# Performance work log

Hardware: AMD Instinct MI355X
Metric: run time of the kernel (lower is better)

## Reference

```python
import jax, jax.numpy as jnp
import numpy as np

NODE_SIZE = 500000
LINK_SIZE = 500
DIM = 128
NORM_P = 1
MARGIN = 1.0
BATCH = 16384


def setup_inputs() -> dict:
    key = jax.random.key(0)
    k1, k2, k3, k4, k5, k6, k7, k8 = jax.random.split(key, 8)
    ur_e = 6.0 / np.sqrt(DIM)
    ur_m = 6.0 / DIM
    node_w = jax.random.uniform(k1, (NODE_SIZE, DIM), jnp.float32, -ur_e, ur_e)
    link_w = jax.random.uniform(k2, (LINK_SIZE, DIM), jnp.float32, -ur_e, ur_e)
    transfer_w = jax.random.uniform(k3, (LINK_SIZE, DIM * DIM), jnp.float32, -ur_m, ur_m)
    sp = jax.random.randint(k4, (BATCH,), 0, NODE_SIZE)
    tp = jax.random.randint(k5, (BATCH,), 0, NODE_SIZE)
    sn = jax.random.randint(k6, (BATCH,), 0, NODE_SIZE)
    tn = jax.random.randint(k7, (BATCH,), 0, NODE_SIZE)
    r = jax.random.randint(k8, (BATCH,), 0, LINK_SIZE)
    return {"node_w": node_w, "link_w": link_w, "transfer_w": transfer_w,
            "sp": sp, "tp": tp, "sn": sn, "tn": tn, "r": r}


def _distance(node_w, link_w, transfer_w, s, r, t):
    # gather embeddings
    s_emb = node_w[s]                      # [B, D]
    t_emb = node_w[t]                      # [B, D]
    r_emb = link_w[r]                      # [B, D]
    M = transfer_w[r].reshape(-1, DIM, DIM)  # [B, D, D]
    # per-sample (1xD)x(DxD) matvec: e @ M
    s_proj = jnp.einsum('bd,bde->be', s_emb, M)
    t_proj = jnp.einsum('bd,bde->be', t_emb, M)
    diff = s_proj + r_emb - t_proj
    if NORM_P == 1:
        return jnp.sum(jnp.abs(diff), axis=1)
    return jnp.sum(jnp.abs(diff) ** NORM_P, axis=1) ** (1.0 / NORM_P)


def reference(node_w, link_w, transfer_w, sp, tp, sn, tn, r):
    pos = _distance(node_w, link_w, transfer_w, sp, r, tp)
    neg = _distance(node_w, link_w, transfer_w, sn, r, tn)
    # MarginRankingLoss with target = -1: max(0, (pos - neg) + margin)
    loss = jnp.maximum(pos - neg + MARGIN, 0.0)
    return jnp.mean(loss)
```

## Files before the change

kernel.cpp:

```cpp
#include <hip/hip_runtime.h>

#define BATCH 16384
#define DIM 128
#define NLINK 500

#define WS_COUNTS 0
#define WS_OFFSETS 512
#define WS_CURSOR 1024
#define WS_BUCKET 1536

__global__ void k_zero(int* wsi, float* out) {
    int t = threadIdx.x;
    wsi[WS_COUNTS + t] = 0;
    if (t == 0) out[0] = 0.0f;
}

__global__ void k_hist(const int* __restrict__ r, int* wsi) {
    int i = blockIdx.x * blockDim.x + threadIdx.x;
    if (i < BATCH) atomicAdd(&wsi[WS_COUNTS + r[i]], 1);
}

__global__ void k_scan(int* wsi) {
    __shared__ int buf[512];
    int t = threadIdx.x;
    int v = (t < NLINK) ? wsi[WS_COUNTS + t] : 0;
    buf[t] = v;
    __syncthreads();
    for (int off = 1; off < 512; off <<= 1) {
        int x = (t >= off) ? buf[t - off] : 0;
        __syncthreads();
        buf[t] += x;
        __syncthreads();
    }
    int excl = buf[t] - v;
    if (t < NLINK) {
        wsi[WS_OFFSETS + t] = excl;
        wsi[WS_CURSOR + t] = excl;
    }
    if (t == 0) wsi[WS_OFFSETS + NLINK] = BATCH;
}

__global__ void k_scatter(const int* __restrict__ r, int* wsi) {
    int i = blockIdx.x * blockDim.x + threadIdx.x;
    if (i < BATCH) {
        int pos = atomicAdd(&wsi[WS_CURSOR + r[i]], 1);
        wsi[WS_BUCKET + pos] = i;
    }
}

__global__ __launch_bounds__(256, 2) void k_main(
    const float* __restrict__ node_w, const float* __restrict__ link_w,
    const float* __restrict__ transfer_w,
    const int* __restrict__ sp, const int* __restrict__ tp,
    const int* __restrict__ sn, const int* __restrict__ tn,
    const int* __restrict__ wsi, float* __restrict__ out)
{
    __shared__ float Ms[DIM * DIM];
    __shared__ float dp[8][DIM];
    __shared__ float dn[8][DIM];
    __shared__ float remb[DIM];
    __shared__ float wred[4];

    const int link = blockIdx.x;
    const int t = threadIdx.x;

    {
        const float4* g = (const float4*)(transfer_w + (size_t)link * (DIM * DIM));
        float4* s = (float4*)Ms;
        #pragma unroll
        for (int i = 0; i < 16; i++) s[t + 256 * i] = g[t + 256 * i];
    }
    if (t < 32) ((float4*)remb)[t] = ((const float4*)(link_w + link * DIM))[t];

    const int begin = wsi[WS_OFFSETS + link];
    const int end   = wsi[WS_OFFSETS + link + 1];
    const int sub = t >> 5;
    const int q   = t & 31;

    float loss_acc = 0.0f;
    __syncthreads();

    for (int k = begin; k < end; k += 8) {
        const int myk = k + sub;
        const bool active = (myk < end);
        if (active) {
            int b = wsi[WS_BUCKET + myk];
            const float4* a = (const float4*)(node_w + (size_t)sp[b] * DIM);
            const float4* c = (const float4*)(node_w + (size_t)tp[b] * DIM);
            float4 av = a[q], cv = c[q];
            float4 rp; rp.x = av.x - cv.x; rp.y = av.y - cv.y;
                       rp.z = av.z - cv.z; rp.w = av.w - cv.w;
            ((float4*)dp[sub])[q] = rp;
            const float4* e2 = (const float4*)(node_w + (size_t)sn[b] * DIM);
            const float4* f2 = (const float4*)(node_w + (size_t)tn[b] * DIM);
            float4 ev = e2[q], fv = f2[q];
            float4 rn; rn.x = ev.x - fv.x; rn.y = ev.y - fv.y;
                       rn.z = ev.z - fv.z; rn.w = ev.w - fv.w;
            ((float4*)dn[sub])[q] = rn;
        }
        __syncthreads();

        float4 accp = {0.f, 0.f, 0.f, 0.f};
        float4 accn = {0.f, 0.f, 0.f, 0.f};
        const float4* dpr = (const float4*)dp[sub];
        const float4* dnr = (const float4*)dn[sub];
        const float4* M4 = (const float4*)Ms;
        #pragma unroll 4
        for (int d4 = 0; d4 < 32; d4++) {
            float4 vp = dpr[d4];
            float4 vn = dnr[d4];
            float4 m0 = M4[(4 * d4 + 0) * 32 + q];
            float4 m1 = M4[(4 * d4 + 1) * 32 + q];
            float4 m2 = M4[(4 * d4 + 2) * 32 + q];
            float4 m3 = M4[(4 * d4 + 3) * 32 + q];
            accp.x = fmaf(m0.x, vp.x, accp.x); accp.y = fmaf(m0.y, vp.x, accp.y);
            accp.z = fmaf(m0.z, vp.x, accp.z); accp.w = fmaf(m0.w, vp.x, accp.w);
            accn.x = fmaf(m0.x, vn.x, accn.x); accn.y = fmaf(m0.y, vn.x, accn.y);
            accn.z = fmaf(m0.z, vn.x, accn.z); accn.w = fmaf(m0.w, vn.x, accn.w);
            accp.x = fmaf(m1.x, vp.y, accp.x); accp.y = fmaf(m1.y, vp.y, accp.y);
            accp.z = fmaf(m1.z, vp.y, accp.z); accp.w = fmaf(m1.w, vp.y, accp.w);
            accn.x = fmaf(m1.x, vn.y, accn.x); accn.y = fmaf(m1.y, vn.y, accn.y);
            accn.z = fmaf(m1.z, vn.y, accn.z); accn.w = fmaf(m1.w, vn.y, accn.w);
            accp.x = fmaf(m2.x, vp.z, accp.x); accp.y = fmaf(m2.y, vp.z, accp.y);
            accp.z = fmaf(m2.z, vp.z, accp.z); accp.w = fmaf(m2.w, vp.z, accp.w);
            accn.x = fmaf(m2.x, vn.z, accn.x); accn.y = fmaf(m2.y, vn.z, accn.y);
            accn.z = fmaf(m2.z, vn.z, accn.z); accn.w = fmaf(m2.w, vn.z, accn.w);
            accp.x = fmaf(m3.x, vp.w, accp.x); accp.y = fmaf(m3.y, vp.w, accp.y);
            accp.z = fmaf(m3.z, vp.w, accp.z); accp.w = fmaf(m3.w, vp.w, accp.w);
            accn.x = fmaf(m3.x, vn.w, accn.x); accn.y = fmaf(m3.y, vn.w, accn.y);
            accn.z = fmaf(m3.z, vn.w, accn.z); accn.w = fmaf(m3.w, vn.w, accn.w);
        }

        float4 re = ((const float4*)remb)[q];
        float lp = fabsf(accp.x + re.x) + fabsf(accp.y + re.y) +
                   fabsf(accp.z + re.z) + fabsf(accp.w + re.w);
        float ln = fabsf(accn.x + re.x) + fabsf(accn.y + re.y) +
                   fabsf(accn.z + re.z) + fabsf(accn.w + re.w);
        #pragma unroll
        for (int o = 16; o >= 1; o >>= 1) {
            lp += __shfl_xor(lp, o, 64);
            ln += __shfl_xor(ln, o, 64);
        }
        if (q == 0 && active) loss_acc += fmaxf(lp - ln + 1.0f, 0.0f);
        __syncthreads();
    }

    #pragma unroll
    for (int o = 32; o >= 1; o >>= 1) loss_acc += __shfl_xor(loss_acc, o, 64);
    if ((t & 63) == 0) wred[t >> 6] = loss_acc;
    __syncthreads();
    if (t == 0) {
        float s = wred[0] + wred[1] + wred[2] + wred[3];
        atomicAdd(out, s * (1.0f / BATCH));
    }
}

extern "C" void kernel_launch(void* const* d_in, const int* in_sizes, int n_in,
                              void* d_out, int out_size, void* d_ws, size_t ws_size,
                              hipStream_t stream) {
    const float* node_w     = (const float*)d_in[0];
    const float* link_w     = (const float*)d_in[1];
    const float* transfer_w = (const float*)d_in[2];
    const int* sp = (const int*)d_in[3];
    const int* tp = (const int*)d_in[4];
    const int* sn = (const int*)d_in[5];
    const int* tn = (const int*)d_in[6];
    const int* r  = (const int*)d_in[7];
    float* out = (float*)d_out;
    int* wsi = (int*)d_ws;

    k_zero<<<1, 512, 0, stream>>>(wsi, out);
    k_hist<<<(BATCH + 255) / 256, 256, 0, stream>>>(r, wsi);
    k_scan<<<1, 512, 0, stream>>>(wsi);
    k_scatter<<<(BATCH + 255) / 256, 256, 0, stream>>>(r, wsi);
    k_main<<<NLINK, 256, 0, stream>>>(node_w, link_w, transfer_w,
                                      sp, tp, sn, tn, wsi, out);
}
```

Baseline: 363.7 us.

## Split each link's output columns across two blocks with per-sample atomic partial norms

Each link is now processed by two blocks, each owning half of the 128 output columns. Each block stages only a 128x64 slice of the transfer matrix in LDS, so there are 1000 blocks with three allowed per CU instead of 500 with two. The L1 partial sums for positive and negative samples are atomically accumulated into per-sample workspace arrays, and a new final kernel applies the hinge and takes the mean. The cost is that each sample's node rows are now gathered twice, and the change adds global atomics plus an extra zeroing pass and an extra kernel launch.

```diff
diff --git a/kernel.cpp b/kernel.cpp
--- a/kernel.cpp
+++ b/kernel.cpp
@@ -3,16 +3,27 @@
 #define BATCH 16384
 #define DIM 128
 #define NLINK 500
+#define EHALF 64
+#define NS 16
+#define DP_STRIDE 132
 
 #define WS_COUNTS 0
 #define WS_OFFSETS 512
 #define WS_CURSOR 1024
 #define WS_BUCKET 1536
+#define WS_POS (1536 + BATCH)
+#define WS_NEG (WS_POS + BATCH)
+#define NZERO (512 + 2 * BATCH + 1)
 
 __global__ void k_zero(int* wsi, float* out) {
-    int t = threadIdx.x;
-    wsi[WS_COUNTS + t] = 0;
-    if (t == 0) out[0] = 0.0f;
+    int i = blockIdx.x * 256 + threadIdx.x;
+    if (i < 512) {
+        wsi[WS_COUNTS + i] = 0;
+    } else if (i < 512 + 2 * BATCH) {
+        ((float*)(wsi + WS_POS))[i - 512] = 0.0f;
+    } else if (i == 512 + 2 * BATCH) {
+        out[0] = 0.0f;
+    }
 }
 
 __global__ void k_hist(const int* __restrict__ r, int* wsi) {
@@ -48,71 +59,80 @@
     }
 }
 
-__global__ __launch_bounds__(256, 2) void k_main(
+__global__ __launch_bounds__(256, 3) void k_main(
     const float* __restrict__ node_w, const float* __restrict__ link_w,
     const float* __restrict__ transfer_w,
     const int* __restrict__ sp, const int* __restrict__ tp,
     const int* __restrict__ sn, const int* __restrict__ tn,
-    const int* __restrict__ wsi, float* __restrict__ out)
+    int* __restrict__ wsi)
 {
-    __shared__ float Ms[DIM * DIM];
-    __shared__ float dp[8][DIM];
-    __shared__ float dn[8][DIM];
-    __shared__ float remb[DIM];
-    __shared__ float wred[4];
-
-    const int link = blockIdx.x;
+    __shared__ float Ms[DIM * EHALF];
+    __shared__ float dp[NS * DP_STRIDE];
+    __shared__ float dn[NS * DP_STRIDE];
+    __shared__ float remb[EHALF];
+
+    const int link = blockIdx.x >> 1;
+    const int h = blockIdx.x & 1;
     const int t = threadIdx.x;
 
     {
-        const float4* g = (const float4*)(transfer_w + (size_t)link * (DIM * DIM));
-        float4* s = (float4*)Ms;
+        const float4* G = (const float4*)transfer_w;
+        float4* Ms4 = (float4*)Ms;
         #pragma unroll
-        for (int i = 0; i < 16; i++) s[t + 256 * i] = g[t + 256 * i];
-    }
-    if (t < 32) ((float4*)remb)[t] = ((const float4*)(link_w + link * DIM))[t];
+        for (int i = 0; i < 8; i++) {
+            int c = t + 256 * i;
+            Ms4[c] = G[link * 4096 + (c >> 4) * 32 + h * 16 + (c & 15)];
+        }
+    }
+    if (t < 16)
+        ((float4*)remb)[t] = ((const float4*)(link_w + link * DIM + h * EHALF))[t];
 
     const int begin = wsi[WS_OFFSETS + link];
     const int end   = wsi[WS_OFFSETS + link + 1];
-    const int sub = t >> 5;
-    const int q   = t & 31;
-
-    float loss_acc = 0.0f;
+    const int g = t >> 4;
+    const int q = t & 15;
+    float* dpr = dp + g * DP_STRIDE;
+    float* dnr = dn + g * DP_STRIDE;
+    float* posF = (float*)(wsi + WS_POS);
+    float* negF = (float*)(wsi + WS_NEG);
+
     __syncthreads();
 
-    for (int k = begin; k < end; k += 8) {
-        const int myk = k + sub;
+    for (int k = begin; k < end; k += NS) {
+        const int myk = k + g;
         const bool active = (myk < end);
+        int b = 0;
         if (active) {
-            int b = wsi[WS_BUCKET + myk];
-            const float4* a = (const float4*)(node_w + (size_t)sp[b] * DIM);
-            const float4* c = (const float4*)(node_w + (size_t)tp[b] * DIM);
-            float4 av = a[q], cv = c[q];
-            float4 rp; rp.x = av.x - cv.x; rp.y = av.y - cv.y;
-                       rp.z = av.z - cv.z; rp.w = av.w - cv.w;
-            ((float4*)dp[sub])[q] = rp;
+            b = wsi[WS_BUCKET + myk];
+            const float4* a  = (const float4*)(node_w + (size_t)sp[b] * DIM);
+            const float4* c2 = (const float4*)(node_w + (size_t)tp[b] * DIM);
+            float4 a0 = a[q], a1 = a[q + 16], c0 = c2[q], c1 = c2[q + 16];
+            float4 w0, w1;
+            w0.x = a0.x - c0.x; w0.y = a0.y - c0.y; w0.z = a0.z - c0.z; w0.w = a0.w - c0.w;
+            w1.x = a1.x - c1.x; w1.y = a1.y - c1.y; w1.z = a1.z - c1.z; w1.w = a1.w - c1.w;
+            ((float4*)dpr)[q] = w0;
+            ((float4*)dpr)[q + 16] = w1;
             const float4* e2 = (const float4*)(node_w + (size_t)sn[b] * DIM);
             const float4* f2 = (const float4*)(node_w + (size_t)tn[b] * DIM);
-            float4 ev = e2[q], fv = f2[q];
-            float4 rn; rn.x = ev.x - fv.x; rn.y = ev.y - fv.y;
-                       rn.z = ev.z - fv.z; rn.w = ev.w - fv.w;
-            ((float4*)dn[sub])[q] = rn;
+            float4 e0 = e2[q], e1 = e2[q + 16], f0 = f2[q], f1 = f2[q + 16];
+            w0.x = e0.x - f0.x; w0.y = e0.y - f0.y; w0.z = e0.z - f0.z; w0.w = e0.w - f0.w;
+            w1.x = e1.x - f1.x; w1.y = e1.y - f1.y; w1.z = e1.z - f1.z; w1.w = e1.w - f1.w;
+            ((float4*)dnr)[q] = w0;
+            ((float4*)dnr)[q + 16] = w1;
         }
         __syncthreads();
 
         float4 accp = {0.f, 0.f, 0.f, 0.f};
         float4 accn = {0.f, 0.f, 0.f, 0.f};
-        const float4* dpr = (const float4*)dp[sub];
-        const float4* dnr = (const float4*)dn[sub];
         const float4* M4 = (const float4*)Ms;
         #pragma unroll 4
         for (int d4 = 0; d4 < 32; d4++) {
-            float4 vp = dpr[d4];
-            float4 vn = dnr[d4];
-            float4 m0 = M4[(4 * d4 + 0) * 32 + q];
-            float4 m1 = M4[(4 * d4 + 1) * 32 + q];
-            float4 m2 = M4[(4 * d4 + 2) * 32 + q];
-            float4 m3 = M4[(4 * d4 + 3) * 32 + q];
+            float4 vp = ((const float4*)dpr)[d4];
+            float4 vn = ((const float4*)dnr)[d4];
+            float4 m0 = M4[(4 * d4 + 0) * 16 + q];
+            float4 m1 = M4[(4 * d4 + 1) * 16 + q];
+            float4 m2 = M4[(4 * d4 + 2) * 16 + q];
+            float4 m3 = M4[(4 * d4 + 3) * 16 + q];
             accp.x = fmaf(m0.x, vp.x, accp.x); accp.y = fmaf(m0.y, vp.x, accp.y);
             accp.z = fmaf(m0.z, vp.x, accp.z); accp.w = fmaf(m0.w, vp.x, accp.w);
             accn.x = fmaf(m0.x, vn.x, accn.x); accn.y = fmaf(m0.y, vn.x, accn.y);
@@ -137,22 +157,31 @@
         float ln = fabsf(accn.x + re.x) + fabsf(accn.y + re.y) +
                    fabsf(accn.z + re.z) + fabsf(accn.w + re.w);
         #pragma unroll
-        for (int o = 16; o >= 1; o >>= 1) {
-            lp += __shfl_xor(lp, o, 64);
-            ln += __shfl_xor(ln, o, 64);
-        }
-        if (q == 0 && active) loss_acc += fmaxf(lp - ln + 1.0f, 0.0f);
-        __syncthreads();
-    }
-
+        for (int o = 8; o >= 1; o >>= 1) {
+            lp += __shfl_xor(lp, o, 16);
+            ln += __shfl_xor(ln, o, 16);
+        }
+        if (active && q == 0) {
+            atomicAdd(&posF[b], lp);
+            atomicAdd(&negF[b], ln);
+        }
+        __syncthreads();
+    }
+}
+
+__global__ void k_final(const int* __restrict__ wsi, float* __restrict__ out) {
+    const float* posF = (const float*)(wsi + WS_POS);
+    const float* negF = (const float*)(wsi + WS_NEG);
+    int i = blockIdx.x * 256 + threadIdx.x;
+    float l = 0.0f;
+    if (i < BATCH) l = fmaxf(posF[i] - negF[i] + 1.0f, 0.0f);
     #pragma unroll
-    for (int o = 32; o >= 1; o >>= 1) loss_acc += __shfl_xor(loss_acc, o, 64);
-    if ((t & 63) == 0) wred[t >> 6] = loss_acc;
+    for (int o = 32; o >= 1; o >>= 1) l += __shfl_xor(l, o, 64);
+    __shared__ float w[4];
+    if ((threadIdx.x & 63) == 0) w[threadIdx.x >> 6] = l;
     __syncthreads();
-    if (t == 0) {
-        float s = wred[0] + wred[1] + wred[2] + wred[3];
-        atomicAdd(out, s * (1.0f / BATCH));
-    }
+    if (threadIdx.x == 0)
+        atomicAdd(out, (w[0] + w[1] + w[2] + w[3]) * (1.0f / BATCH));
 }
 
 extern "C" void kernel_launch(void* const* d_in, const int* in_sizes, int n_in,
@@ -169,10 +198,11 @@
     float* out = (float*)d_out;
     int* wsi = (int*)d_ws;
 
-    k_zero<<<1, 512, 0, stream>>>(wsi, out);
+    k_zero<<<(NZERO + 255) / 256, 256, 0, stream>>>(wsi, out);
     k_hist<<<(BATCH + 255) / 256, 256, 0, stream>>>(r, wsi);
     k_scan<<<1, 512, 0, stream>>>(wsi);
     k_scatter<<<(BATCH + 255) / 256, 256, 0, stream>>>(r, wsi);
-    k_main<<<NLINK, 256, 0, stream>>>(node_w, link_w, transfer_w,
-                                      sp, tp, sn, tn, wsi, out);
-}
+    k_main<<<NLINK * 2, 256, 0, stream>>>(node_w, link_w, transfer_w,
+                                          sp, tp, sn, tn, wsi);
+    k_final<<<(BATCH + 255) / 256, 256, 0, stream>>>(wsi, out);
+}
```

New measurement: 359.0 us. Within noise of the previous version (-1.3%).
